# Optimization experiments

Measured on AMD Instinct MI355X. Metric: run time of the kernel, lower is better.

## Reference

```python
import jax, jax.numpy as jnp
import numpy as np

EMBED = 1024
HEADS = 16
HEAD_DIM = EMBED // HEADS
WINDOW = 256

def _linear(x, W, b):
    # torch nn.Linear: y = x @ W.T + b, W shape (out, in)
    return jnp.einsum('bse,oe->bso', x, W) + b

def setup_inputs() -> dict:
    key = jax.random.key(0)
    ks = jax.random.split(key, 16)
    B, S = 2, 2048
    std = 1.0 / np.sqrt(EMBED)
    d = {
        'query': jax.random.normal(ks[0], (B, S, EMBED), jnp.float32),
        'key':   jax.random.normal(ks[1], (B, S, EMBED), jnp.float32),
        'value': jax.random.normal(ks[2], (B, S, EMBED), jnp.float32),
        'Wq': jax.random.normal(ks[3], (EMBED, EMBED), jnp.float32) * std,
        'bq': jnp.zeros((EMBED,), jnp.float32),
        'Wk': jax.random.normal(ks[4], (EMBED, EMBED), jnp.float32) * std,
        'bk': jnp.zeros((EMBED,), jnp.float32),
        'Wv': jax.random.normal(ks[5], (EMBED, EMBED), jnp.float32) * std,
        'bv': jnp.zeros((EMBED,), jnp.float32),
        'Wo': jax.random.normal(ks[6], (EMBED, EMBED), jnp.float32) * std,
        'bo': jnp.zeros((EMBED,), jnp.float32),
    }
    return d

def reference(query, key, value, Wq, bq, Wk, bk, Wv, bv, Wo, bo):
    B, S, E = query.shape
    q = _linear(query, Wq, bq)
    k = _linear(key, Wk, bk)
    v = _linear(value, Wv, bv)
    # (B, H, S, D)
    q = q.reshape(B, S, HEADS, HEAD_DIM).transpose(0, 2, 1, 3)
    k = k.reshape(B, S, HEADS, HEAD_DIM).transpose(0, 2, 1, 3)
    v = v.reshape(B, S, HEADS, HEAD_DIM).transpose(0, 2, 1, 3)
    scale = 1.0 / jnp.sqrt(jnp.asarray(HEAD_DIM, q.dtype))
    scores = jnp.einsum('bhqd,bhkd->bhqk', q, k) * scale
    # Faithful local masking: mask is 0 inside window [i-w//2, i+w//2], 1 outside,
    # and is ADDED to scores (as in the source, not -inf fill).
    i = jnp.arange(S)[:, None]
    j = jnp.arange(S)[None, :]
    half = WINDOW // 2
    band = (jnp.abs(i - j) <= half)
    add_mask = jnp.where(band, 0.0, 1.0).astype(scores.dtype)  # (S, S)
    scores = scores + add_mask[None, None, :, :]
    attn = jax.nn.softmax(scores, axis=-1)  # dropout = identity (eval)
    out = jnp.einsum('bhqk,bhkd->bhqd', attn, v)
    out = out.transpose(0, 2, 1, 3).reshape(B, S, E)
    return _linear(out, Wo, bo)
```

## Files before the change

### kernel.cpp

```cpp
#include <hip/hip_runtime.h>
#include <stdint.h>

#define B_ 2
#define S_ 2048
#define E_ 1024
#define H_ 16
#define D_ 64
#define M_ (B_*S_)
#define PROJ_ ((size_t)M_*E_)
#define HALF_W 128

typedef float    f32x4 __attribute__((ext_vector_type(4)));
typedef short    s16x4 __attribute__((ext_vector_type(4)));
typedef short    s16x8 __attribute__((ext_vector_type(8)));
typedef __bf16   bf16x8 __attribute__((ext_vector_type(8)));
typedef _Float16 f16x8 __attribute__((ext_vector_type(8)));
typedef unsigned int u32x4 __attribute__((ext_vector_type(4)));

typedef const __attribute__((address_space(1))) void* gas_t;
typedef __attribute__((address_space(3))) void*       las_t;

__device__ __forceinline__ void gl16(const void* g, void* l) {
    __builtin_amdgcn_global_load_lds((gas_t)g, (las_t)l, 16, 0, 0);
}

__device__ __forceinline__ f32x4 MFMA(bf16x8 a, bf16x8 b, f32x4 c) {
    return __builtin_amdgcn_mfma_f32_16x16x32_bf16(a, b, c, 0, 0, 0);
}
__device__ __forceinline__ f32x4 MFMAH(f16x8 a, f16x8 b, f32x4 c) {
    return __builtin_amdgcn_mfma_f32_16x16x32_f16(a, b, c, 0, 0, 0);
}

__device__ __forceinline__ float fexp2(float x) {
    return __builtin_amdgcn_exp2f(x);
}

__device__ __forceinline__ unsigned short f2bf(float f) {
    union { float f; unsigned int u; } x; x.f = f;
    unsigned int u = x.u + 0x7FFFu + ((x.u >> 16) & 1u);
    return (unsigned short)(u >> 16);
}

__device__ __forceinline__ s16x8 cvt8(f32x4 a, f32x4 b) {
    s16x8 h;
    h[0]=(short)f2bf(a[0]); h[1]=(short)f2bf(a[1]); h[2]=(short)f2bf(a[2]); h[3]=(short)f2bf(a[3]);
    h[4]=(short)f2bf(b[0]); h[5]=(short)f2bf(b[1]); h[6]=(short)f2bf(b[2]); h[7]=(short)f2bf(b[3]);
    return h;
}

__global__ __launch_bounds__(256) void cvt_kernel(
    const float* __restrict__ q, const float* __restrict__ k, const float* __restrict__ v,
    const float* __restrict__ Wq, const float* __restrict__ Wk,
    const float* __restrict__ Wv, const float* __restrict__ Wo,
    unsigned short* __restrict__ xq, unsigned short* __restrict__ xk,
    unsigned short* __restrict__ xv, unsigned short* __restrict__ wbf)
{
    const int z = blockIdx.y;
    if (z >= 3 && blockIdx.x >= 512) return;
    const float* src; unsigned short* dst;
    switch (z) {
        case 0: src = q;  dst = xq; break;
        case 1: src = k;  dst = xk; break;
        case 2: src = v;  dst = xv; break;
        case 3: src = Wq; dst = wbf; break;
        case 4: src = Wk; dst = wbf + (size_t)E_*E_; break;
        case 5: src = Wv; dst = wbf + 2*(size_t)E_*E_; break;
        default: src = Wo; dst = wbf + 3*(size_t)E_*E_; break;
    }
    size_t i = ((size_t)blockIdx.x * 256 + threadIdx.x) * 8;
    f32x4 a = *(const f32x4*)(src + i);
    f32x4 c = *(const f32x4*)(src + i + 4);
    *(s16x8*)(dst + i) = cvt8(a, c);
}

__global__ __launch_bounds__(256, 3) void qkv_kernel(
    const unsigned short* __restrict__ xq, const unsigned short* __restrict__ xk,
    const unsigned short* __restrict__ xv,
    const unsigned short* __restrict__ wbf,
    const float* __restrict__ Wq, const float* __restrict__ Wk, const float* __restrict__ Wv,
    const float* __restrict__ bq, const float* __restrict__ bk, const float* __restrict__ bv,
    unsigned short* __restrict__ qkvout)
{
    const int z = blockIdx.z;
    const unsigned short* X  = (z==0) ? xq : (z==1) ? xk : xv;
    const float*          Wf = (z==0) ? Wq : (z==1) ? Wk : Wv;
    const float*        bias = (z==0) ? bq : (z==1) ? bk : bv;
    const unsigned short* Wb = wbf ? (wbf + (size_t)z * E_ * E_) : nullptr;
    unsigned short* dst = qkvout + (size_t)z * PROJ_;

    __shared__ __align__(16) unsigned short As[2][128 * 32];
    __shared__ __align__(16) unsigned short Bs[2][128 * 32];

    const int t = threadIdx.x;
    const int lane = t & 63, w = t >> 6;
    const int quad = lane >> 4, l16 = lane & 15;
    const int wo = (w & 1) * 64, wsb = (w >> 1) * 64;
    const int oBase = blockIdx.x * 128, sBase = blockIdx.y * 128;

    const int r0 = t >> 2;
    const int c4 = (t & 3) ^ (r0 & 3);
    const unsigned short* gX  = X + (size_t)(sBase + r0) * E_ + c4 * 8;
    const unsigned short* gWb = Wb ? Wb + (size_t)(oBase + r0) * E_ + c4 * 8 : nullptr;
    const float*          gWf = Wf + (size_t)(oBase + r0) * E_ + c4 * 8;

    f32x4 acc[4][4] = {};

    auto issue = [&](int kk, int pb) {
        unsigned short* dB = &Bs[pb][(size_t)w * 512];
        gl16(gX + kk, dB);
        gl16(gX + (size_t)64 * E_ + kk, dB + 2048);
        if (gWb) {
            unsigned short* dA = &As[pb][(size_t)w * 512];
            gl16(gWb + kk, dA);
            gl16(gWb + (size_t)64 * E_ + kk, dA + 2048);
        } else {
            const float* gp0 = gWf + kk;
            const float* gp1 = gWf + (size_t)64 * E_ + kk;
            f32x4 a0 = *(const f32x4*)gp0, a1 = *(const f32x4*)(gp0 + 4);
            f32x4 b0 = *(const f32x4*)gp1, b1 = *(const f32x4*)(gp1 + 4);
            *(s16x8*)&As[pb][(size_t)r0 * 32 + (t & 3) * 8]        = cvt8(a0, a1);
            *(s16x8*)&As[pb][(size_t)(r0 + 64) * 32 + (t & 3) * 8] = cvt8(b0, b1);
        }
    };

    issue(0, 0);
    __syncthreads();

    for (int s = 0; s < 32; s++) {
        const int pb = s & 1;
        if (s < 31) issue((s + 1) * 32, pb ^ 1);

        bf16x8 af[4], bfr[4];
        #pragma unroll
        for (int io = 0; io < 4; io++) {
            int r = wo + io * 16 + l16;
            af[io] = *(const bf16x8*)&As[pb][(size_t)r * 32 + ((quad ^ (l16 & 3)) * 8)];
        }
        #pragma unroll
        for (int is = 0; is < 4; is++) {
            int r = wsb + is * 16 + l16;
            bfr[is] = *(const bf16x8*)&Bs[pb][(size_t)r * 32 + ((quad ^ (l16 & 3)) * 8)];
        }
        #pragma unroll
        for (int io = 0; io < 4; io++)
            #pragma unroll
            for (int is = 0; is < 4; is++)
                acc[io][is] = MFMA(af[io], bfr[is], acc[io][is]);
        __syncthreads();
    }

    const float KSCL = 0.1803368801111204f;
    #pragma unroll
    for (int is = 0; is < 4; is++) {
        int sg = sBase + wsb + is * 16 + l16;
        int b = sg >> 11, sg2 = sg & 2047;
        int k6 = sg2 & 63;
        int slot = ((k6 >> 5) & 1) * 32 + ((k6 >> 2) & 3) * 8
                 + ((k6 >> 4) & 1) * 4 + (k6 & 3);
        #pragma unroll
        for (int io = 0; io < 4; io++) {
            int ocol0 = oBase + wo + io * 16 + quad * 4;
            f32x4 bias4 = *(const f32x4*)&bias[ocol0];
            int h = ocol0 >> 6, d0 = ocol0 & 63;
            size_t base = ((size_t)(b * H_ + h)) * ((size_t)S_ * D_);
            if (z == 0) {
                s16x4 h4;
                #pragma unroll
                for (int r = 0; r < 4; r++) h4[r] = (short)f2bf(acc[io][is][r] + bias4[r]);
                *(s16x4*)&dst[base + (size_t)sg2 * D_ + d0] = h4;
            } else if (z == 1) {
                s16x4 h4;
                #pragma unroll
                for (int r = 0; r < 4; r++)
                    h4[r] = (short)f2bf((acc[io][is][r] + bias4[r]) * KSCL);
                *(s16x4*)&dst[base + (size_t)sg2 * D_ + d0] = h4;
            } else {
                size_t vb = base + (size_t)(sg2 >> 6) * 4096 + (size_t)d0 * 64 + slot;
                #pragma unroll
                for (int r = 0; r < 4; r++) {
                    _Float16 hv = (_Float16)(acc[io][is][r] + bias4[r]);
                    dst[vb + (size_t)r * 64] = __builtin_bit_cast(unsigned short, hv);
                }
            }
        }
    }
}

__global__ __launch_bounds__(256, 2) void attn_kernel(
    const unsigned short* __restrict__ qkvout, unsigned short* __restrict__ attnout)
{
    const int bh = blockIdx.x, b = bh >> 4, h = bh & 15;
    const int qbase = blockIdx.y * 128;
    const int t = threadIdx.x, w = t >> 6, lane = t & 63;
    const int quad = lane >> 4, l16 = lane & 15;

    const unsigned short* qgp = qkvout + (size_t)bh * (S_ * D_);
    const unsigned short* kg = qkvout + PROJ_ + (size_t)bh * (S_ * D_);
    const unsigned short* vT = qkvout + 2 * PROJ_ + (size_t)bh * (S_ * D_);

    __shared__ __align__(16) unsigned short Ks [2][64 * 64];
    __shared__ __align__(16) unsigned short VTs[2][64 * 64];

    const int qw = qbase + w * 32;
    bf16x8 aq[2][2];
    #pragma unroll
    for (int qg = 0; qg < 2; qg++) {
        int qi = qw + qg * 16 + l16;
        aq[qg][0] = *(const bf16x8*)&qgp[(size_t)qi * 64 + quad * 8];
        aq[qg][1] = *(const bf16x8*)&qgp[(size_t)qi * 64 + 32 + quad * 8];
    }

    f32x4 O[2][4] = {};
    f32x4 Sd[2] = {};

    const int r0 = t >> 3;
    const int ch = ((t & 7) ^ (r0 & 7)) * 8;

    f16x8 onesv;
    #pragma unroll
    for (int j = 0; j < 8; j++) onesv[j] = (_Float16)1.0f;

    const float LOG2E = 1.44269504089f;
    const f32x4 one4 = {LOG2E, LOG2E, LOG2E, LOG2E};
    const f32x4 zero4 = {};

    auto issue = [&](int kt, int pb) {
        unsigned short* dK = &Ks [pb][(size_t)w * 512];
        unsigned short* dV = &VTs[pb][(size_t)w * 512];
        gl16(kg + (size_t)(kt + r0) * 64 + ch,      dK);
        gl16(kg + (size_t)(kt + r0 + 32) * 64 + ch, dK + 2048);
        gl16(vT + (size_t)(kt + r0) * 64 + ch,      dV);
        gl16(vT + (size_t)(kt + r0 + 32) * 64 + ch, dV + 2048);
    };

    issue(0, 0);
    __syncthreads();

    #pragma unroll 2
    for (int s = 0; s < 32; s++) {
        const int pb = s & 1;
        const int kt = s * 64;
        if (s < 31) issue(kt + 64, pb ^ 1);

        int cls[2];
        #pragma unroll
        for (int qg = 0; qg < 2; qg++) {
            int d = qw + qg * 16 - kt;
            cls[qg] = (d >= -64 && d <= 112) ? 0 : ((d >= 192 || d <= -144) ? 1 : 2);
        }

        const int sw = l16 & 7;
        u32x4 up[2][2];
        #pragma unroll
        for (int sub = 0; sub < 4; sub++) {
            int row = sub * 16 + l16;
            bf16x8 bk0 = *(const bf16x8*)&Ks[pb][(size_t)row * 64 + ((quad ^ sw) * 8)];
            bf16x8 bk1 = *(const bf16x8*)&Ks[pb][(size_t)row * 64 + (((4 + quad) ^ sw) * 8)];
            #pragma unroll
            for (int qg = 0; qg < 2; qg++) {
                f32x4 ci;
                if (cls[qg] == 0) {
                    ci = zero4;
                } else if (cls[qg] == 1) {
                    ci = one4;
                } else {
                    int jb = kt + sub * 16 + quad * 4;
                    int qi = qw + qg * 16 + l16;
                    #pragma unroll
                    for (int r = 0; r < 4; r++) {
                        int di = qi - (jb + r); di = di < 0 ? -di : di;
                        ci[r] = (di <= HALF_W) ? 0.f : LOG2E;
                    }
                }
                f32x4 zz = MFMA(bk0, aq[qg][0], ci);
                zz = MFMA(bk1, aq[qg][1], zz);
                float p0 = fexp2(zz[0]), p1 = fexp2(zz[1]);
                float p2 = fexp2(zz[2]), p3 = fexp2(zz[3]);
                up[qg][sub >> 1][(sub & 1) * 2 + 0] =
                    __builtin_bit_cast(unsigned int, __builtin_amdgcn_cvt_pkrtz(p0, p1));
                up[qg][sub >> 1][(sub & 1) * 2 + 1] =
                    __builtin_bit_cast(unsigned int, __builtin_amdgcn_cvt_pkrtz(p2, p3));
            }
        }
        f16x8 aP[2][2];
        aP[0][0] = __builtin_bit_cast(f16x8, up[0][0]);
        aP[0][1] = __builtin_bit_cast(f16x8, up[0][1]);
        aP[1][0] = __builtin_bit_cast(f16x8, up[1][0]);
        aP[1][1] = __builtin_bit_cast(f16x8, up[1][1]);

        #pragma unroll
        for (int dt = 0; dt < 4; dt++) {
            int row = dt * 16 + l16;
            f16x8 v0 = *(const f16x8*)&VTs[pb][(size_t)row * 64 + ((quad ^ sw) * 8)];
            f16x8 v1 = *(const f16x8*)&VTs[pb][(size_t)row * 64 + (((4 + quad) ^ sw) * 8)];
            #pragma unroll
            for (int qg = 0; qg < 2; qg++) {
                O[qg][dt] = MFMAH(aP[qg][0], v0, O[qg][dt]);
                O[qg][dt] = MFMAH(aP[qg][1], v1, O[qg][dt]);
            }
        }
        #pragma unroll
        for (int qg = 0; qg < 2; qg++) {
            Sd[qg] = MFMAH(aP[qg][0], onesv, Sd[qg]);
            Sd[qg] = MFMAH(aP[qg][1], onesv, Sd[qg]);
        }
        __syncthreads();
    }

    #pragma unroll
    for (int qg = 0; qg < 2; qg++) {
        float rd[4];
        #pragma unroll
        for (int r = 0; r < 4; r++) rd[r] = 1.0f / Sd[qg][r];
        #pragma unroll
        for (int dt = 0; dt < 4; dt++)
            #pragma unroll
            for (int r = 0; r < 4; r++) {
                float oo = O[qg][dt][r] * rd[r];
                int srow2 = qw + qg * 16 + quad * 4 + r;
                int col   = h * 64 + dt * 16 + l16;
                attnout[((size_t)(b * S_ + srow2)) * E_ + col] = f2bf(oo);
            }
    }
}

__global__ __launch_bounds__(256, 2) void oproj_kernel(
    const unsigned short* __restrict__ Aattn, const unsigned short* __restrict__ WoBf,
    const float* __restrict__ Wo, const float* __restrict__ bo, float* __restrict__ out)
{
    __shared__ __align__(16) unsigned short As[2][64 * 32];
    __shared__ __align__(16) unsigned short Bs[2][128 * 32];

    const int t = threadIdx.x;
    const int lane = t & 63, w = t >> 6;
    const int quad = lane >> 4, l16 = lane & 15;
    const int wm = (w & 1) * 32, wn = (w >> 1) * 64;
    const int rowBase = blockIdx.y * 64, nBase = blockIdx.x * 128;

    const int r0 = t >> 2;
    const int c4 = (t & 3) ^ (r0 & 3);
    const unsigned short* gA  = Aattn + (size_t)(rowBase + r0) * E_ + c4 * 8;
    const unsigned short* gBb = WoBf ? WoBf + (size_t)(nBase + r0) * E_ + c4 * 8 : nullptr;
    const float*          gBf = Wo + (size_t)(nBase + r0) * E_ + c4 * 8;

    f32x4 acc[2][4] = {};

    auto issue = [&](int kk, int pb) {
        gl16(gA + kk, &As[pb][(size_t)w * 512]);
        if (gBb) {
            unsigned short* dB = &Bs[pb][(size_t)w * 512];
            gl16(gBb + kk, dB);
            gl16(gBb + (size_t)64 * E_ + kk, dB + 2048);
        } else {
            const float* gp0 = gBf + kk;
            const float* gp1 = gBf + (size_t)64 * E_ + kk;
            f32x4 a0 = *(const f32x4*)gp0, a1 = *(const f32x4*)(gp0 + 4);
            f32x4 b0 = *(const f32x4*)gp1, b1 = *(const f32x4*)(gp1 + 4);
            *(s16x8*)&Bs[pb][(size_t)r0 * 32 + (t & 3) * 8]        = cvt8(a0, a1);
            *(s16x8*)&Bs[pb][(size_t)(r0 + 64) * 32 + (t & 3) * 8] = cvt8(b0, b1);
        }
    };

    issue(0, 0);
    __syncthreads();

    for (int s = 0; s < 32; s++) {
        const int pb = s & 1;
        if (s < 31) issue((s + 1) * 32, pb ^ 1);

        bf16x8 af[2], bfr[4];
        #pragma unroll
        for (int im = 0; im < 2; im++) {
            int r = wm + im * 16 + l16;
            af[im] = *(const bf16x8*)&As[pb][(size_t)r * 32 + ((quad ^ (l16 & 3)) * 8)];
        }
        #pragma unroll
        for (int in = 0; in < 4; in++) {
            int r = wn + in * 16 + l16;
            bfr[in] = *(const bf16x8*)&Bs[pb][(size_t)r * 32 + ((quad ^ (l16 & 3)) * 8)];
        }
        #pragma unroll
        for (int im = 0; im < 2; im++)
            #pragma unroll
            for (int in = 0; in < 4; in++)
                acc[im][in] = MFMA(af[im], bfr[in], acc[im][in]);
        __syncthreads();
    }

    #pragma unroll
    for (int im = 0; im < 2; im++)
      #pragma unroll
      for (int in = 0; in < 4; in++) {
          int col = nBase + wn + in * 16 + l16;
          float bb = bo[col];
          #pragma unroll
          for (int r = 0; r < 4; r++) {
              int row = rowBase + wm + im * 16 + quad * 4 + r;
              out[(size_t)row * E_ + col] = acc[im][in][r] + bb;
          }
      }
}

extern "C" void kernel_launch(void* const* d_in, const int* in_sizes, int n_in,
                              void* d_out, int out_size, void* d_ws, size_t ws_size,
                              hipStream_t stream) {
    const float* query = (const float*)d_in[0];
    const float* key_  = (const float*)d_in[1];
    const float* value = (const float*)d_in[2];
    const float* Wq = (const float*)d_in[3];
    const float* bq = (const float*)d_in[4];
    const float* Wk = (const float*)d_in[5];
    const float* bk = (const float*)d_in[6];
    const float* Wv = (const float*)d_in[7];
    const float* bv = (const float*)d_in[8];
    const float* Wo = (const float*)d_in[9];
    const float* bo = (const float*)d_in[10];

    unsigned short* ws      = (unsigned short*)d_ws;
    unsigned short* xv      = ws;
    unsigned short* attnout = ws;
    unsigned short* qkvout  = ws + PROJ_;
    size_t needW = (4 * PROJ_ + 4 * (size_t)E_ * E_) * 2;
    unsigned short* wbf = (ws_size >= needW) ? (ws + 4 * PROJ_) : nullptr;
    unsigned short* xq = (unsigned short*)d_out;
    unsigned short* xk = xq + PROJ_;

    cvt_kernel<<<dim3(2048, wbf ? 7 : 3), 256, 0, stream>>>(
        query, key_, value, Wq, Wk, Wv, Wo, xq, xk, xv, wbf);
    qkv_kernel<<<dim3(8, 32, 3), 256, 0, stream>>>(
        xq, xk, xv, wbf, Wq, Wk, Wv, bq, bk, bv, qkvout);
    attn_kernel<<<dim3(32, 16), 256, 0, stream>>>(qkvout, attnout);
    oproj_kernel<<<dim3(8, 64), 256, 0, stream>>>(
        attnout, wbf ? wbf + 3 * (size_t)E_ * E_ : nullptr, Wo, bo, (float*)d_out);
}
```

Before: 226.7 us.

## Split attention waves across key halves with LDS reduction and smaller query blocks

Each attention block now covers 64 queries instead of 128, with its four waves arranged as two query halves by two key halves of each 64-key tile. Partial outputs and softmax denominators from the second key half are combined through shared memory before normalising and writing. The grid doubles and launch bounds allow four blocks per CU, aiming for higher occupancy and latency hiding. The cost is twice the K/V loading per query and an extra end-of-kernel reduction and barrier.

After: 222.5 us. Within noise of the previous version (-1.8%).

```diff
diff --git a/kernel.cpp b/kernel.cpp
--- a/kernel.cpp
+++ b/kernel.cpp
@@ -186,13 +186,15 @@
     }
 }
 
-__global__ __launch_bounds__(256, 2) void attn_kernel(
+__global__ __launch_bounds__(256, 4) void attn_kernel(
     const unsigned short* __restrict__ qkvout, unsigned short* __restrict__ attnout)
 {
     const int bh = blockIdx.x, b = bh >> 4, h = bh & 15;
-    const int qbase = blockIdx.y * 128;
+    const int qbase = blockIdx.y * 64;
     const int t = threadIdx.x, w = t >> 6, lane = t & 63;
     const int quad = lane >> 4, l16 = lane & 15;
+    const int qh = w & 1;
+    const int hw = w >> 1;
 
     const unsigned short* qgp = qkvout + (size_t)bh * (S_ * D_);
     const unsigned short* kg = qkvout + PROJ_ + (size_t)bh * (S_ * D_);
@@ -201,7 +203,7 @@
     __shared__ __align__(16) unsigned short Ks [2][64 * 64];
     __shared__ __align__(16) unsigned short VTs[2][64 * 64];
 
-    const int qw = qbase + w * 32;
+    const int qw = qbase + qh * 32;
     bf16x8 aq[2][2];
     #pragma unroll
     for (int qg = 0; qg < 2; qg++) {
@@ -236,35 +238,31 @@
     issue(0, 0);
     __syncthreads();
 
+    const int sw = l16 & 7;
+    const int vch = (((hw * 4) + quad) ^ sw) * 8;
+
     #pragma unroll 2
     for (int s = 0; s < 32; s++) {
         const int pb = s & 1;
         const int kt = s * 64;
         if (s < 31) issue(kt + 64, pb ^ 1);
 
-        int cls[2];
-        #pragma unroll
-        for (int qg = 0; qg < 2; qg++) {
-            int d = qw + qg * 16 - kt;
-            cls[qg] = (d >= -64 && d <= 112) ? 0 : ((d >= 192 || d <= -144) ? 1 : 2);
-        }
-
-        const int sw = l16 & 7;
-        u32x4 up[2][2];
-        #pragma unroll
-        for (int sub = 0; sub < 4; sub++) {
-            int row = sub * 16 + l16;
+        f32x4 pp[2][2];
+        #pragma unroll
+        for (int sub = 0; sub < 2; sub++) {
+            int row = hw * 32 + sub * 16 + l16;
             bf16x8 bk0 = *(const bf16x8*)&Ks[pb][(size_t)row * 64 + ((quad ^ sw) * 8)];
             bf16x8 bk1 = *(const bf16x8*)&Ks[pb][(size_t)row * 64 + (((4 + quad) ^ sw) * 8)];
             #pragma unroll
             for (int qg = 0; qg < 2; qg++) {
+                int d = qw + qg * 16 - (kt + hw * 32 + sub * 16);
                 f32x4 ci;
-                if (cls[qg] == 0) {
+                if (d >= -112 && d <= 112) {
                     ci = zero4;
-                } else if (cls[qg] == 1) {
+                } else if (d >= 144 || d <= -144) {
                     ci = one4;
                 } else {
-                    int jb = kt + sub * 16 + quad * 4;
+                    int jb = kt + hw * 32 + sub * 16 + quad * 4;
                     int qi = qw + qg * 16 + l16;
                     #pragma unroll
                     for (int r = 0; r < 4; r++) {
@@ -274,53 +272,66 @@
                 }
                 f32x4 zz = MFMA(bk0, aq[qg][0], ci);
                 zz = MFMA(bk1, aq[qg][1], zz);
-                float p0 = fexp2(zz[0]), p1 = fexp2(zz[1]);
-                float p2 = fexp2(zz[2]), p3 = fexp2(zz[3]);
-                up[qg][sub >> 1][(sub & 1) * 2 + 0] =
-                    __builtin_bit_cast(unsigned int, __builtin_amdgcn_cvt_pkrtz(p0, p1));
-                up[qg][sub >> 1][(sub & 1) * 2 + 1] =
-                    __builtin_bit_cast(unsigned int, __builtin_amdgcn_cvt_pkrtz(p2, p3));
+                pp[qg][sub][0] = fexp2(zz[0]); pp[qg][sub][1] = fexp2(zz[1]);
+                pp[qg][sub][2] = fexp2(zz[2]); pp[qg][sub][3] = fexp2(zz[3]);
             }
         }
-        f16x8 aP[2][2];
-        aP[0][0] = __builtin_bit_cast(f16x8, up[0][0]);
-        aP[0][1] = __builtin_bit_cast(f16x8, up[0][1]);
-        aP[1][0] = __builtin_bit_cast(f16x8, up[1][0]);
-        aP[1][1] = __builtin_bit_cast(f16x8, up[1][1]);
+
+        f16x8 aP[2];
+        #pragma unroll
+        for (int qg = 0; qg < 2; qg++) {
+            u32x4 up;
+            up[0] = __builtin_bit_cast(unsigned int, __builtin_amdgcn_cvt_pkrtz(pp[qg][0][0], pp[qg][0][1]));
+            up[1] = __builtin_bit_cast(unsigned int, __builtin_amdgcn_cvt_pkrtz(pp[qg][0][2], pp[qg][0][3]));
+            up[2] = __builtin_bit_cast(unsigned int, __builtin_amdgcn_cvt_pkrtz(pp[qg][1][0], pp[qg][1][1]));
+            up[3] = __builtin_bit_cast(unsigned int, __builtin_amdgcn_cvt_pkrtz(pp[qg][1][2], pp[qg][1][3]));
+            aP[qg] = __builtin_bit_cast(f16x8, up);
+        }
 
         #pragma unroll
         for (int dt = 0; dt < 4; dt++) {
             int row = dt * 16 + l16;
-            f16x8 v0 = *(const f16x8*)&VTs[pb][(size_t)row * 64 + ((quad ^ sw) * 8)];
-            f16x8 v1 = *(const f16x8*)&VTs[pb][(size_t)row * 64 + (((4 + quad) ^ sw) * 8)];
-            #pragma unroll
-            for (int qg = 0; qg < 2; qg++) {
-                O[qg][dt] = MFMAH(aP[qg][0], v0, O[qg][dt]);
-                O[qg][dt] = MFMAH(aP[qg][1], v1, O[qg][dt]);
+            f16x8 v = *(const f16x8*)&VTs[pb][(size_t)row * 64 + vch];
+            O[0][dt] = MFMAH(aP[0], v, O[0][dt]);
+            O[1][dt] = MFMAH(aP[1], v, O[1][dt]);
+        }
+        Sd[0] = MFMAH(aP[0], onesv, Sd[0]);
+        Sd[1] = MFMAH(aP[1], onesv, Sd[1]);
+        __syncthreads();
+    }
+
+    float* LsO = (float*)&Ks[0][0];
+    float* LsS = (float*)&VTs[0][0];
+    if (hw == 1) {
+        #pragma unroll
+        for (int qg = 0; qg < 2; qg++) {
+            #pragma unroll
+            for (int dt = 0; dt < 4; dt++)
+                *(f32x4*)&LsO[(((qg * 4 + dt) * 128) + qh * 64 + lane) * 4] = O[qg][dt];
+            *(f32x4*)&LsS[((qg * 128) + qh * 64 + lane) * 4] = Sd[qg];
+        }
+    }
+    __syncthreads();
+    if (hw == 0) {
+        #pragma unroll
+        for (int qg = 0; qg < 2; qg++) {
+            f32x4 st = Sd[qg] + *(const f32x4*)&LsS[((qg * 128) + qh * 64 + lane) * 4];
+            float rd[4];
+            #pragma unroll
+            for (int r = 0; r < 4; r++) rd[r] = 1.0f / st[r];
+            #pragma unroll
+            for (int dt = 0; dt < 4; dt++) {
+                f32x4 ot = O[qg][dt]
+                    + *(const f32x4*)&LsO[(((qg * 4 + dt) * 128) + qh * 64 + lane) * 4];
+                #pragma unroll
+                for (int r = 0; r < 4; r++) {
+                    float oo = ot[r] * rd[r];
+                    int srow2 = qw + qg * 16 + quad * 4 + r;
+                    int col   = h * 64 + dt * 16 + l16;
+                    attnout[((size_t)(b * S_ + srow2)) * E_ + col] = f2bf(oo);
+                }
             }
         }
-        #pragma unroll
-        for (int qg = 0; qg < 2; qg++) {
-            Sd[qg] = MFMAH(aP[qg][0], onesv, Sd[qg]);
-            Sd[qg] = MFMAH(aP[qg][1], onesv, Sd[qg]);
-        }
-        __syncthreads();
-    }
-
-    #pragma unroll
-    for (int qg = 0; qg < 2; qg++) {
-        float rd[4];
-        #pragma unroll
-        for (int r = 0; r < 4; r++) rd[r] = 1.0f / Sd[qg][r];
-        #pragma unroll
-        for (int dt = 0; dt < 4; dt++)
-            #pragma unroll
-            for (int r = 0; r < 4; r++) {
-                float oo = O[qg][dt][r] * rd[r];
-                int srow2 = qw + qg * 16 + quad * 4 + r;
-                int col   = h * 64 + dt * 16 + l16;
-                attnout[((size_t)(b * S_ + srow2)) * E_ + col] = f2bf(oo);
-            }
     }
 }
 
@@ -429,7 +440,7 @@
         query, key_, value, Wq, Wk, Wv, Wo, xq, xk, xv, wbf);
     qkv_kernel<<<dim3(8, 32, 3), 256, 0, stream>>>(
         xq, xk, xv, wbf, Wq, Wk, Wv, bq, bk, bv, qkvout);
-    attn_kernel<<<dim3(32, 16), 256, 0, stream>>>(qkvout, attnout);
+    attn_kernel<<<dim3(32, 32), 256, 0, stream>>>(qkvout, attnout);
     oproj_kernel<<<dim3(8, 64), 256, 0, stream>>>(
         attnout, wbf ? wbf + 3 * (size_t)E_ * E_ : nullptr, Wo, bo, (float*)d_out);
 }
```
